# Optimization experiments

Hardware: AMD Instinct MI355X
Metric: run time of the kernel (lower is better)

The kernel has to match this reference:

```python
import jax, jax.numpy as jnp
import numpy as np
from jax import lax

G, NPER, K = 64, 1024, 512          # graphs, nodes per graph, kept per graph (ceil(0.5*1024))
N, E = G * NPER, 1_048_576          # total nodes, total edges
F, H, C = 128, 128, 10              # in_feats, hidden_dim, num_classes


def gcn(x, src, dst, ew, W, b, num_nodes):
    """PyG GCNConv: D^{-1/2}(A+I)D^{-1/2} X W + b, with edge weights ew."""
    xw = x @ W                                              # [N, H]
    deg = jax.ops.segment_sum(ew, dst, num_segments=num_nodes) + 1.0  # +1 self loop
    dinv = lax.rsqrt(deg)
    coef = dinv[src] * dinv[dst] * ew                       # [E]
    agg = jax.ops.segment_sum(coef[:, None] * xw[src], dst, num_segments=num_nodes)
    return agg + (dinv * dinv)[:, None] * xw + b            # self-loop term + bias


def setup_inputs() -> dict:
    key = jax.random.key(0)
    ks = jax.random.split(key, 10)
    x = jax.random.normal(ks[0], (N, F), jnp.float32)
    # intra-graph random edges: dst forced into same graph block as src
    src = jax.random.randint(ks[1], (E,), 0, N, dtype=jnp.int32)
    dst = (src // NPER) * NPER + jax.random.randint(ks[2], (E,), 0, NPER, dtype=jnp.int32)
    edge_index = jnp.stack([src, dst])                      # [2, E]
    batch = jnp.repeat(jnp.arange(G, dtype=jnp.int32), NPER)
    W1 = jax.random.normal(ks[3], (F, H), jnp.float32) / np.sqrt(F)
    b1 = jnp.zeros((H,), jnp.float32)
    p = jax.random.normal(ks[4], (H,), jnp.float32) / np.sqrt(H)   # TopKPooling score vector
    W2 = jax.random.normal(ks[5], (H, H), jnp.float32) / np.sqrt(H)
    b2 = jnp.zeros((H,), jnp.float32)
    Wl = jax.random.normal(ks[6], (H, C), jnp.float32) / np.sqrt(H)
    bl = jnp.zeros((C,), jnp.float32)
    return dict(x=x, edge_index=edge_index, batch=batch, W1=W1, b1=b1, p=p, W2=W2, b2=b2, Wl=Wl, bl=bl)


def reference(x, edge_index, batch, W1, b1, p, W2, b2, Wl, bl):
    src, dst = edge_index[0], edge_index[1]
    ew1 = jnp.ones((E,), x.dtype)
    h = jax.nn.relu(gcn(x, src, dst, ew1, W1, b1, N))       # conv1 + relu

    # --- TopKPooling: score = tanh(x.p/||p||), keep top-K per graph, gate x by score ---
    score = jnp.tanh((h @ p) / jnp.linalg.norm(p))          # [N]
    vals, idx = lax.top_k(score.reshape(G, NPER), K)        # per-graph top-k, [G, K]
    perm = (idx + jnp.arange(G, dtype=idx.dtype)[:, None] * NPER).reshape(-1)  # global ids [G*K]
    h2 = h[perm] * vals.reshape(-1, 1)                      # gated kept nodes [G*K, H]

    # edge re-index: keep only edges with both endpoints surviving (mask via weight 0)
    new_id = jnp.full((N,), -1, jnp.int32).at[perm].set(jnp.arange(G * K, dtype=jnp.int32))
    s2, d2 = new_id[src], new_id[dst]
    mask = (s2 >= 0) & (d2 >= 0)
    ew2 = mask.astype(h.dtype)
    s2 = jnp.where(mask, s2, 0)
    d2 = jnp.where(mask, d2, 0)

    h3 = jax.nn.relu(gcn(h2, s2, d2, ew2, W2, b2, G * K))   # conv2 + relu

    pooled = h3.reshape(G, K, H).mean(axis=1)               # global_mean_pool (equal counts)
    return pooled @ Wl + bl                                 # [G, C]
```

## Files before the change

kernel.cpp:

```cpp
#include <hip/hip_runtime.h>

#define NNODES 65536
#define NEDGES 1048576
#define NGRAPH 64
#define NPERG  1024
#define KEEP   512
#define M2     (NGRAPH * KEEP)
#define HD     128
#define NC     10
#define EMAX   20480

#define OW1 0
#define OW2 16384
#define OWL 32768
#define OB1 34048
#define OB2 34176
#define OP  34304
#define OBL 34432
#define NCVT 34448

typedef __attribute__((ext_vector_type(8))) short bf16x8;
typedef __attribute__((ext_vector_type(4))) float f32x4;

__device__ __forceinline__ float bf2f(unsigned short u) {
    return __uint_as_float(((unsigned int)u) << 16);
}
__device__ __forceinline__ unsigned short f2bf(float f) {
    unsigned int u = __float_as_uint(f);
    unsigned int r = (u + 0x7FFFu + ((u >> 16) & 1u)) >> 16;
    return (unsigned short)r;
}

__global__ __launch_bounds__(256) void prep_kernel(
    const void* __restrict__ W1, const void* __restrict__ b1, const void* __restrict__ p,
    const void* __restrict__ W2, const void* __restrict__ b2, const void* __restrict__ Wl,
    const void* __restrict__ bl, int* __restrict__ flag, float* __restrict__ cw,
    float* __restrict__ invnorm, int* __restrict__ new_id, int* __restrict__ ghist,
    int* __restrict__ gcur0, float* __restrict__ pooled,
    unsigned short* __restrict__ w1t, unsigned short* __restrict__ w2t,
    const int* __restrict__ src, int* __restrict__ phist) {
    int bid = blockIdx.x, t = threadIdx.x;
    const unsigned short* w1u = (const unsigned short*)W1;
    int local = 0;
    for (int i = t; i < 512; i += 256) {
        unsigned short u = w1u[2 * i];
        int e = (u >> 7) & 0xFF;
        local += (e >= 100 && e <= 140) ? 1 : 0;
    }
    __shared__ int red[256];
    __shared__ int lh[NGRAPH];
    red[t] = local;
    __syncthreads();
    for (int off = 128; off; off >>= 1) {
        if (t < off) red[t] += red[t + off];
        __syncthreads();
    }
    int fl = (red[0] >= 384) ? 1 : 0;
    if (bid == 0 && t == 0) flag[0] = fl;

    if (bid < 135) {
        int gid = bid * 256 + t;
        if (gid < NCVT) {
            const void* srcp; int idx;
            if (gid < OB1) {
                if (gid < OW2)      { srcp = W1; idx = gid - OW1; }
                else if (gid < OWL) { srcp = W2; idx = gid - OW2; }
                else                { srcp = Wl; idx = gid - OWL; }
            } else {
                if (gid < OB2)      { srcp = b1; idx = gid - OB1; }
                else if (gid < OP)  { srcp = b2; idx = gid - OB2; }
                else if (gid < OBL) { srcp = p;  idx = gid - OP; }
                else                { srcp = bl; idx = gid - OBL; }
            }
            float v;
            if (gid >= OWL && gid < OB1 && idx >= 1280) v = 0.f;
            else if (gid >= OBL && idx >= NC) v = 0.f;
            else if (fl) v = bf2f(((const unsigned short*)srcp)[idx]);
            else v = ((const float*)srcp)[idx];
            cw[gid] = v;
            if (gid < OW2) {
                int k = gid >> 7, n = gid & 127;
                w1t[n * 128 + k] = f2bf(v);
            } else if (gid < OWL) {
                int r = gid - OW2;
                int k = r >> 7, n = r & 127;
                w2t[n * 128 + k] = f2bf(v);
            }
        }
    } else if (bid == 135) {
        __shared__ float s2a[128];
        float pv = 0.f;
        if (t < 128) pv = fl ? bf2f(((const unsigned short*)p)[t]) : ((const float*)p)[t];
        if (t < 128) s2a[t] = pv * pv;
        __syncthreads();
        for (int off = 64; off; off >>= 1) {
            if (t < off) s2a[t] += s2a[t + off];
            __syncthreads();
        }
        if (t == 0) invnorm[0] = 1.0f / sqrtf(s2a[0]);
    } else if (bid < 392) {
        int i = (bid - 136) * 256 + t;
        new_id[i] = -1;
        if (i < NGRAPH) { ghist[i] = 0; gcur0[i] = 0; }
        if (i < NGRAPH * HD) pooled[i] = 0.f;
    } else {
        if (t < NGRAPH) lh[t] = 0;
        __syncthreads();
        int e0 = (bid - 392) * 4096;
        for (int k = 0; k < 16; k++) atomicAdd(&lh[src[e0 + k * 256 + t] >> 10], 1);
        __syncthreads();
        if (t < NGRAPH) phist[(bid - 392) * 64 + t] = lh[t];
    }
}

__global__ __launch_bounds__(256) void binpass_kernel(const int* __restrict__ src,
                                                      const int* __restrict__ dst,
                                                      const int* __restrict__ phist,
                                                      int* __restrict__ ghist,
                                                      int* __restrict__ gcur0,
                                                      unsigned int* __restrict__ elist) {
    __shared__ int gh[NGRAPH];
    __shared__ int gbS[NGRAPH];
    __shared__ int lh[NGRAPH];
    __shared__ int lbase[NGRAPH];
    __shared__ int qsum[4][NGRAPH];
    int tid = threadIdx.x;
    {
        int g = tid & 63, q = tid >> 6;
        int s = 0;
        for (int b = q * 64; b < q * 64 + 64; b++) s += phist[b * 64 + g];
        qsum[q][g] = s;
    }
    __syncthreads();
    if (tid < NGRAPH) {
        gh[tid] = qsum[0][tid] + qsum[1][tid] + qsum[2][tid] + qsum[3][tid];
        lh[tid] = 0;
        if (blockIdx.x == 0) ghist[tid] = gh[tid];
    }
    __syncthreads();
    if (tid == 0) {
        int s = 0;
        for (int i = 0; i < NGRAPH; i++) { gbS[i] = s; s += gh[i]; }
    }
    __syncthreads();
    int e0 = blockIdx.x * 4096;
    int gs[16]; unsigned int pk[16];
    for (int k = 0; k < 16; k++) {
        int e = e0 + k * 256 + tid;
        int s = src[e], d = dst[e];
        gs[k] = s >> 10;
        pk[k] = (unsigned)(s & 1023) | ((unsigned)(d & 1023) << 10);
        atomicAdd(&lh[gs[k]], 1);
    }
    __syncthreads();
    if (tid < NGRAPH) { lbase[tid] = gbS[tid] + atomicAdd(&gcur0[tid], lh[tid]); lh[tid] = 0; }
    __syncthreads();
    for (int k = 0; k < 16; k++) {
        int g = gs[k];
        int pos = lbase[g] + atomicAdd(&lh[g], 1);
        elist[pos] = pk[k];
    }
}

__global__ __launch_bounds__(1024) void g1csr_kernel(
    const unsigned int* __restrict__ elist, const int* __restrict__ ghist,
    unsigned short* __restrict__ csr16, int* __restrict__ node_base,
    int* __restrict__ deg_out, float* __restrict__ dinv_out,
    const void* __restrict__ Araw, const unsigned short* __restrict__ Wtb,
    unsigned int* __restrict__ Cb, const int* __restrict__ flag) {
    __shared__ unsigned short sc[EMAX];
    __shared__ int cnt[NPERG];
    __shared__ int cur[NPERG];
    __shared__ int wsum[16];
    __shared__ int gh[NGRAPH];
    __shared__ int baseS, nS;
    int bid = blockIdx.x, t = threadIdx.x;
    if (bid < NGRAPH) {
        int g = bid;
        cnt[t] = 0;
        if (t < NGRAPH) gh[t] = ghist[t];
        __syncthreads();
        if (t == 0) {
            int s = 0;
            for (int i = 0; i < g; i++) s += gh[i];
            baseS = s; nS = gh[g];
        }
        __syncthreads();
        int base = baseS;
        int n = nS; if (n > EMAX) n = EMAX;
        for (int j = t; j < n; j += 1024) atomicAdd(&cnt[(elist[base + j] >> 10) & 1023], 1);
        __syncthreads();
        int v = cnt[t];
        int lane = t & 63;
        int x = v;
        for (int off = 1; off < 64; off <<= 1) {
            int y = __shfl_up(x, off);
            if (lane >= off) x += y;
        }
        if (lane == 63) wsum[t >> 6] = x;
        __syncthreads();
        if (t < 16) {
            int wv = wsum[t];
            int wx = wv;
            for (int off = 1; off < 16; off <<= 1) {
                int y = __shfl_up(wx, off);
                if (t >= off) wx += y;
            }
            wsum[t] = wx - wv;
        }
        __syncthreads();
        int excl = x - v + wsum[t >> 6];
        cur[t] = excl;
        deg_out[g * NPERG + t] = v;
        dinv_out[g * NPERG + t] = rsqrtf((float)v + 1.0f);
        node_base[g * NPERG + t] = base + excl;
        __syncthreads();
        for (int j = t; j < n; j += 1024) {
            unsigned int pk = elist[base + j];
            int d = (pk >> 10) & 1023;
            int pos = atomicAdd(&cur[d], 1);
            sc[pos] = (unsigned short)(pk & 1023);
        }
        __syncthreads();
        for (int j = t; j < n; j += 1024) csr16[base + j] = sc[j];
        return;
    }
    int row0 = (bid - NGRAPH) * 256;
    int wave = t >> 6, lane = t & 63;
    int r0 = row0 + wave * 16;
    int row = r0 + (lane & 15);
    int ko = (lane >> 4) * 8;
    f32x4 acc[8];
#pragma unroll
    for (int c = 0; c < 8; c++) acc[c] = (f32x4){0.f, 0.f, 0.f, 0.f};
    bf16x8 afr[4];
    if (flag[0]) {
        const unsigned short* arow = (const unsigned short*)Araw + (size_t)row * HD + ko;
#pragma unroll
        for (int kk = 0; kk < 4; kk++) afr[kk] = *(const bf16x8*)(arow + kk * 32);
    } else {
        const float* arow = (const float*)Araw + (size_t)row * HD + ko;
#pragma unroll
        for (int kk = 0; kk < 4; kk++) {
            float4 f0 = *(const float4*)(arow + kk * 32);
            float4 f1 = *(const float4*)(arow + kk * 32 + 4);
            bf16x8 a;
            a[0] = (short)f2bf(f0.x); a[1] = (short)f2bf(f0.y);
            a[2] = (short)f2bf(f0.z); a[3] = (short)f2bf(f0.w);
            a[4] = (short)f2bf(f1.x); a[5] = (short)f2bf(f1.y);
            a[6] = (short)f2bf(f1.z); a[7] = (short)f2bf(f1.w);
            afr[kk] = a;
        }
    }
    const unsigned short* brow = Wtb + (lane & 15) * HD + ko;
#pragma unroll
    for (int kk = 0; kk < 4; kk++) {
#pragma unroll
        for (int c = 0; c < 8; c++) {
            bf16x8 b = *(const bf16x8*)(brow + c * 16 * HD + kk * 32);
            acc[c] = __builtin_amdgcn_mfma_f32_16x16x32_bf16(afr[kk], b, acc[c], 0, 0, 0);
        }
    }
    int orow0 = r0 + (lane >> 4) * 4;
    bool even = !(lane & 1);
#pragma unroll
    for (int c = 0; c < 8; c++) {
#pragma unroll
        for (int j = 0; j < 4; j++) {
            float v = acc[c][j];
            float pt = __shfl_xor(v, 1);
            if (even) {
                unsigned int u = (unsigned int)f2bf(v) | ((unsigned int)f2bf(pt) << 16);
                Cb[(size_t)(orow0 + j) * 64 + ((c * 16 + (lane & 15)) >> 1)] = u;
            }
        }
    }
}

__global__ __launch_bounds__(256) void s1_pull(const unsigned short* __restrict__ csr16,
                                               const int* __restrict__ node_base,
                                               const int* __restrict__ deg,
                                               const float* __restrict__ dinv,
                                               const unsigned int* __restrict__ xwb,
                                               const float* __restrict__ b1,
                                               const float* __restrict__ pvec,
                                               const float* __restrict__ invnorm,
                                               unsigned int* __restrict__ hb,
                                               float* __restrict__ score) {
    int b = blockIdx.x;
    int xcd = b & 7, j = b >> 3;
    int g = (j >> 8) * 8 + xcd;
    int n = g * NPERG + (j & 255) * 4 + (threadIdx.x >> 6);
    int lane = threadIdx.x & 63;
    int gb = g * NPERG;
    int base = node_base[n], cnt = deg[n];
    int e = 0; float ds = 0.f;
    if (lane < cnt) {
        e = csr16[base + lane];
        ds = dinv[gb + e];
    }
    float a0 = 0.f, a1 = 0.f;
    int klim = cnt < 64 ? cnt : 64;
    int k = 0;
    for (; k + 7 < klim; k += 8) {
        int s0 = __shfl(e, k),     s1 = __shfl(e, k + 1);
        int s2 = __shfl(e, k + 2), s3 = __shfl(e, k + 3);
        int s4 = __shfl(e, k + 4), s5 = __shfl(e, k + 5);
        int s6 = __shfl(e, k + 6), s7 = __shfl(e, k + 7);
        float d0 = __shfl(ds, k),     d1 = __shfl(ds, k + 1);
        float d2 = __shfl(ds, k + 2), d3 = __shfl(ds, k + 3);
        float d4 = __shfl(ds, k + 4), d5 = __shfl(ds, k + 5);
        float d6 = __shfl(ds, k + 6), d7 = __shfl(ds, k + 7);
        unsigned int u0 = xwb[(size_t)(gb + s0) * 64 + lane];
        unsigned int u1 = xwb[(size_t)(gb + s1) * 64 + lane];
        unsigned int u2 = xwb[(size_t)(gb + s2) * 64 + lane];
        unsigned int u3 = xwb[(size_t)(gb + s3) * 64 + lane];
        unsigned int u4 = xwb[(size_t)(gb + s4) * 64 + lane];
        unsigned int u5 = xwb[(size_t)(gb + s5) * 64 + lane];
        unsigned int u6 = xwb[(size_t)(gb + s6) * 64 + lane];
        unsigned int u7 = xwb[(size_t)(gb + s7) * 64 + lane];
        a0 += d0 * __uint_as_float(u0 << 16); a1 += d0 * __uint_as_float(u0 & 0xFFFF0000u);
        a0 += d1 * __uint_as_float(u1 << 16); a1 += d1 * __uint_as_float(u1 & 0xFFFF0000u);
        a0 += d2 * __uint_as_float(u2 << 16); a1 += d2 * __uint_as_float(u2 & 0xFFFF0000u);
        a0 += d3 * __uint_as_float(u3 << 16); a1 += d3 * __uint_as_float(u3 & 0xFFFF0000u);
        a0 += d4 * __uint_as_float(u4 << 16); a1 += d4 * __uint_as_float(u4 & 0xFFFF0000u);
        a0 += d5 * __uint_as_float(u5 << 16); a1 += d5 * __uint_as_float(u5 & 0xFFFF0000u);
        a0 += d6 * __uint_as_float(u6 << 16); a1 += d6 * __uint_as_float(u6 & 0xFFFF0000u);
        a0 += d7 * __uint_as_float(u7 << 16); a1 += d7 * __uint_as_float(u7 & 0xFFFF0000u);
    }
    for (; k + 3 < klim; k += 4) {
        int s0 = __shfl(e, k), s1 = __shfl(e, k + 1);
        int s2 = __shfl(e, k + 2), s3 = __shfl(e, k + 3);
        float d0 = __shfl(ds, k), d1 = __shfl(ds, k + 1);
        float d2 = __shfl(ds, k + 2), d3 = __shfl(ds, k + 3);
        unsigned int u0 = xwb[(size_t)(gb + s0) * 64 + lane];
        unsigned int u1 = xwb[(size_t)(gb + s1) * 64 + lane];
        unsigned int u2 = xwb[(size_t)(gb + s2) * 64 + lane];
        unsigned int u3 = xwb[(size_t)(gb + s3) * 64 + lane];
        a0 += d0 * __uint_as_float(u0 << 16); a1 += d0 * __uint_as_float(u0 & 0xFFFF0000u);
        a0 += d1 * __uint_as_float(u1 << 16); a1 += d1 * __uint_as_float(u1 & 0xFFFF0000u);
        a0 += d2 * __uint_as_float(u2 << 16); a1 += d2 * __uint_as_float(u2 & 0xFFFF0000u);
        a0 += d3 * __uint_as_float(u3 << 16); a1 += d3 * __uint_as_float(u3 & 0xFFFF0000u);
    }
    for (; k < klim; k++) {
        int sk = __shfl(e, k);
        float dk = __shfl(ds, k);
        unsigned int u = xwb[(size_t)(gb + sk) * 64 + lane];
        a0 += dk * __uint_as_float(u << 16); a1 += dk * __uint_as_float(u & 0xFFFF0000u);
    }
    for (; k < cnt; k++) {
        int sk = csr16[base + k];
        float dk = dinv[gb + sk];
        unsigned int u = xwb[(size_t)(gb + sk) * 64 + lane];
        a0 += dk * __uint_as_float(u << 16); a1 += dk * __uint_as_float(u & 0xFFFF0000u);
    }
    float dn = dinv[n];
    float self = dn * dn;
    unsigned int us = xwb[(size_t)n * 64 + lane];
    float2 bb = ((const float2*)b1)[lane];
    float h0 = fmaxf(dn * a0 + self * __uint_as_float(us << 16) + bb.x, 0.f);
    float h1 = fmaxf(dn * a1 + self * __uint_as_float(us & 0xFFFF0000u) + bb.y, 0.f);
    hb[(size_t)n * 64 + lane] = (unsigned int)f2bf(h0) | ((unsigned int)f2bf(h1) << 16);
    float2 pp = ((const float2*)pvec)[lane];
    float sv = h0 * pp.x + h1 * pp.y;
    for (int off = 32; off; off >>= 1) sv += __shfl_down(sv, off);
    if (lane == 0) score[n] = tanhf(sv * invnorm[0]);
}

__global__ __launch_bounds__(1024) void topk_kernel(const float* __restrict__ score,
                                                    float* __restrict__ vals,
                                                    int* __restrict__ perm,
                                                    int* __restrict__ new_id) {
    __shared__ float sv[1024];
    __shared__ int si[1024];
    int g = blockIdx.x, t = threadIdx.x;
    float v = score[g * NPERG + t];
    int idx = t;
    for (int k = 2; k <= 1024; k <<= 1) {
        for (int j = k >> 1; j > 0; j >>= 1) {
            bool desc = ((t & k) == 0);
            bool up = (t & j) != 0;
            float vb; int ib;
            if (j >= 64) {
                sv[t] = v; si[t] = idx;
                __syncthreads();
                vb = sv[t ^ j]; ib = si[t ^ j];
                bool cmp = (v > vb) || (v == vb && idx < ib);
                bool keep = up ? (cmp != desc) : (cmp == desc);
                if (!keep) { v = vb; idx = ib; }
                __syncthreads();
            } else {
                vb = __shfl_xor(v, j);
                ib = __shfl_xor(idx, j);
                bool cmp = (v > vb) || (v == vb && idx < ib);
                bool keep = up ? (cmp != desc) : (cmp == desc);
                if (!keep) { v = vb; idx = ib; }
            }
        }
    }
    if (t < KEEP) {
        int node = g * NPERG + idx;
        int slot = g * KEEP + t;
        vals[slot] = v;
        perm[slot] = node;
        new_id[node] = slot;
    }
}

__global__ __launch_bounds__(512) void g2deg_kernel(
    const unsigned int* __restrict__ elist, const int* __restrict__ ghist,
    const int* __restrict__ new_id, float* __restrict__ dinv2,
    const unsigned int* __restrict__ hb, const int* __restrict__ perm,
    const float* __restrict__ vals, const unsigned short* __restrict__ Wtb,
    unsigned int* __restrict__ Cb) {
    __shared__ int d2[KEEP];
    __shared__ int gh[NGRAPH];
    __shared__ int baseS, nS;
    int bid = blockIdx.x, t = threadIdx.x;
    if (bid < NGRAPH) {
        int g = bid;
        if (t < KEEP) d2[t] = 0;
        if (t < NGRAPH) gh[t] = ghist[t];
        __syncthreads();
        if (t == 0) {
            int s = 0;
            for (int i = 0; i < g; i++) s += gh[i];
            baseS = s; nS = gh[g];
        }
        __syncthreads();
        int base = baseS, n = nS;
        int gb = g * NPERG;
        int kb = g * KEEP;
        for (int j = t; j < n; j += 512) {
            unsigned int pk = elist[base + j];
            int s = pk & 1023, d = (pk >> 10) & 1023;
            int ns = new_id[gb + s], nd = new_id[gb + d];
            if (ns >= 0 && nd >= 0) atomicAdd(&d2[nd - kb], 1);
        }
        __syncthreads();
        if (t < KEEP) dinv2[kb + t] = rsqrtf((float)d2[t] + 1.0f);
        return;
    }
    int row0 = (bid - NGRAPH) * 128;
    int wave = t >> 6, lane = t & 63;
    int r0 = row0 + wave * 16;
    int m = r0 + (lane & 15);
    int ko = (lane >> 4) * 8;
    float sc = vals[m];
    const unsigned int* arow = hb + (size_t)perm[m] * 64 + (ko >> 1);
    bf16x8 afr[4];
#pragma unroll
    for (int kk = 0; kk < 4; kk++) {
        uint4 q = *(const uint4*)(arow + kk * 16);
        bf16x8 a;
        a[0] = (short)f2bf(bf2f((unsigned short)q.x) * sc);
        a[1] = (short)f2bf(bf2f((unsigned short)(q.x >> 16)) * sc);
        a[2] = (short)f2bf(bf2f((unsigned short)q.y) * sc);
        a[3] = (short)f2bf(bf2f((unsigned short)(q.y >> 16)) * sc);
        a[4] = (short)f2bf(bf2f((unsigned short)q.z) * sc);
        a[5] = (short)f2bf(bf2f((unsigned short)(q.z >> 16)) * sc);
        a[6] = (short)f2bf(bf2f((unsigned short)q.w) * sc);
        a[7] = (short)f2bf(bf2f((unsigned short)(q.w >> 16)) * sc);
        afr[kk] = a;
    }
    f32x4 acc[8];
#pragma unroll
    for (int c = 0; c < 8; c++) acc[c] = (f32x4){0.f, 0.f, 0.f, 0.f};
    const unsigned short* brow = Wtb + (lane & 15) * HD + ko;
#pragma unroll
    for (int kk = 0; kk < 4; kk++) {
#pragma unroll
        for (int c = 0; c < 8; c++) {
            bf16x8 b = *(const bf16x8*)(brow + c * 16 * HD + kk * 32);
            acc[c] = __builtin_amdgcn_mfma_f32_16x16x32_bf16(afr[kk], b, acc[c], 0, 0, 0);
        }
    }
    int orow0 = r0 + (lane >> 4) * 4;
    bool even = !(lane & 1);
#pragma unroll
    for (int c = 0; c < 8; c++) {
#pragma unroll
        for (int j = 0; j < 4; j++) {
            float v = acc[c][j];
            float pt = __shfl_xor(v, 1);
            if (even) {
                unsigned int u = (unsigned int)f2bf(v) | ((unsigned int)f2bf(pt) << 16);
                Cb[(size_t)(orow0 + j) * 64 + ((c * 16 + (lane & 15)) >> 1)] = u;
            }
        }
    }
}

__global__ __launch_bounds__(256) void s2_pull(const unsigned short* __restrict__ csr16,
                                               const int* __restrict__ node_base,
                                               const int* __restrict__ deg,
                                               const int* __restrict__ perm,
                                               const int* __restrict__ new_id,
                                               const float* __restrict__ dinv2,
                                               const unsigned int* __restrict__ xwb2,
                                               const float* __restrict__ b2,
                                               float* __restrict__ pooled) {
    __shared__ float pr[HD];
    __shared__ int cnk[4][64];
    __shared__ float cds[4][64];
    int tid = threadIdx.x;
    if (tid < HD) pr[tid] = 0.f;
    __syncthreads();
    int b = blockIdx.x;
    int xcd = b & 7, j = b >> 3;
    int g = (j >> 7) * 8 + xcd;
    int wv = tid >> 6;
    int m = g * KEEP + (j & 127) * 4 + wv;
    int lane = tid & 63;
    int node = perm[m];
    int gb = node & ~(NPERG - 1);
    int base = node_base[node], cnt = deg[node];
    int nk = 0; float ds = 0.f;
    if (lane < cnt) {
        int ns = new_id[gb + csr16[base + lane]];
        if (ns >= 0) { nk = ns; ds = dinv2[ns]; }
    }
    unsigned long long msk = __ballot(ds != 0.f);
    int pos = __popcll(msk & ((1ull << lane) - 1ull));
    if (ds != 0.f) { cnk[wv][pos] = nk; cds[wv][pos] = ds; }
    int na = __popcll(msk);
    float a0 = 0.f, a1 = 0.f;
    int k = 0;
    for (; k + 7 < na; k += 8) {
        int s0 = cnk[wv][k],     s1 = cnk[wv][k + 1];
        int s2 = cnk[wv][k + 2], s3 = cnk[wv][k + 3];
        int s4 = cnk[wv][k + 4], s5 = cnk[wv][k + 5];
        int s6 = cnk[wv][k + 6], s7 = cnk[wv][k + 7];
        float d0 = cds[wv][k],     d1 = cds[wv][k + 1];
        float d2 = cds[wv][k + 2], d3 = cds[wv][k + 3];
        float d4 = cds[wv][k + 4], d5 = cds[wv][k + 5];
        float d6 = cds[wv][k + 6], d7 = cds[wv][k + 7];
        unsigned int u0 = xwb2[(size_t)s0 * 64 + lane];
        unsigned int u1 = xwb2[(size_t)s1 * 64 + lane];
        unsigned int u2 = xwb2[(size_t)s2 * 64 + lane];
        unsigned int u3 = xwb2[(size_t)s3 * 64 + lane];
        unsigned int u4 = xwb2[(size_t)s4 * 64 + lane];
        unsigned int u5 = xwb2[(size_t)s5 * 64 + lane];
        unsigned int u6 = xwb2[(size_t)s6 * 64 + lane];
        unsigned int u7 = xwb2[(size_t)s7 * 64 + lane];
        a0 += d0 * __uint_as_float(u0 << 16); a1 += d0 * __uint_as_float(u0 & 0xFFFF0000u);
        a0 += d1 * __uint_as_float(u1 << 16); a1 += d1 * __uint_as_float(u1 & 0xFFFF0000u);
        a0 += d2 * __uint_as_float(u2 << 16); a1 += d2 * __uint_as_float(u2 & 0xFFFF0000u);
        a0 += d3 * __uint_as_float(u3 << 16); a1 += d3 * __uint_as_float(u3 & 0xFFFF0000u);
        a0 += d4 * __uint_as_float(u4 << 16); a1 += d4 * __uint_as_float(u4 & 0xFFFF0000u);
        a0 += d5 * __uint_as_float(u5 << 16); a1 += d5 * __uint_as_float(u5 & 0xFFFF0000u);
        a0 += d6 * __uint_as_float(u6 << 16); a1 += d6 * __uint_as_float(u6 & 0xFFFF0000u);
        a0 += d7 * __uint_as_float(u7 << 16); a1 += d7 * __uint_as_float(u7 & 0xFFFF0000u);
    }
    for (; k + 3 < na; k += 4) {
        int s0 = cnk[wv][k], s1 = cnk[wv][k + 1];
        int s2 = cnk[wv][k + 2], s3 = cnk[wv][k + 3];
        float d0 = cds[wv][k], d1 = cds[wv][k + 1];
        float d2 = cds[wv][k + 2], d3 = cds[wv][k + 3];
        unsigned int u0 = xwb2[(size_t)s0 * 64 + lane];
        unsigned int u1 = xwb2[(size_t)s1 * 64 + lane];
        unsigned int u2 = xwb2[(size_t)s2 * 64 + lane];
        unsigned int u3 = xwb2[(size_t)s3 * 64 + lane];
        a0 += d0 * __uint_as_float(u0 << 16); a1 += d0 * __uint_as_float(u0 & 0xFFFF0000u);
        a0 += d1 * __uint_as_float(u1 << 16); a1 += d1 * __uint_as_float(u1 & 0xFFFF0000u);
        a0 += d2 * __uint_as_float(u2 << 16); a1 += d2 * __uint_as_float(u2 & 0xFFFF0000u);
        a0 += d3 * __uint_as_float(u3 << 16); a1 += d3 * __uint_as_float(u3 & 0xFFFF0000u);
    }
    for (; k < na; k++) {
        int sk = cnk[wv][k];
        float dk = cds[wv][k];
        unsigned int u = xwb2[(size_t)sk * 64 + lane];
        a0 += dk * __uint_as_float(u << 16); a1 += dk * __uint_as_float(u & 0xFFFF0000u);
    }
    for (int kk = 64; kk < cnt; kk++) {
        int ns = new_id[gb + csr16[base + kk]];
        if (ns >= 0) {
            float dk = dinv2[ns];
            unsigned int u = xwb2[(size_t)ns * 64 + lane];
            a0 += dk * __uint_as_float(u << 16); a1 += dk * __uint_as_float(u & 0xFFFF0000u);
        }
    }
    float dn = dinv2[m];
    float self = dn * dn;
    unsigned int us = xwb2[(size_t)m * 64 + lane];
    float2 bb = ((const float2*)b2)[lane];
    float o0 = fmaxf(dn * a0 + self * __uint_as_float(us << 16) + bb.x, 0.f);
    float o1 = fmaxf(dn * a1 + self * __uint_as_float(us & 0xFFFF0000u) + bb.y, 0.f);
    atomicAdd(&pr[lane * 2], o0);
    atomicAdd(&pr[lane * 2 + 1], o1);
    __syncthreads();
    if (tid < HD) atomicAdd(&pooled[g * HD + tid], pr[tid]);
}

__global__ __launch_bounds__(128) void outk_kernel(const float* __restrict__ pooled,
                                                   const float* __restrict__ Wl,
                                                   const float* __restrict__ bl,
                                                   void* __restrict__ outv,
                                                   const int* __restrict__ flag) {
    int g = blockIdx.x, t = threadIdx.x;
    __shared__ float sp[HD];
    sp[t] = pooled[g * HD + t] * (1.0f / KEEP);
    __syncthreads();
    if (t < NC) {
        float acc = bl[t];
        for (int hh = 0; hh < HD; hh++) acc += sp[hh] * Wl[hh * NC + t];
        if (flag[0]) ((unsigned short*)outv)[g * NC + t] = f2bf(acc);
        else         ((float*)outv)[g * NC + t] = acc;
    }
}

extern "C" void kernel_launch(void* const* d_in, const int* in_sizes, int n_in,
                              void* d_out, int out_size, void* d_ws, size_t ws_size,
                              hipStream_t stream) {
    const int* ei   = (const int*)d_in[1];
    const int* srcv = ei;
    const int* dstv = ei + NEDGES;

    char* w = (char*)d_ws;
    const size_t MB = 1u << 20;
    const size_t KB = 1024;
    float* dinv1     = (float*)(w + 0);
    float* score     = (float*)(w + 256 * KB);
    float* vals      = (float*)(w + 512 * KB);
    int*   perm      = (int*)(w + 640 * KB);
    int*   new_id    = (int*)(w + 768 * KB);
    int*   deg1      = (int*)(w + 1024 * KB);
    int*   node_base = (int*)(w + 1280 * KB);
    float* dinv2     = (float*)(w + 1536 * KB);
    float* invnorm   = (float*)(w + 1664 * KB);
    int*   flag      = (int*)(w + 1664 * KB + 64);
    int*   ghist     = (int*)(w + 1664 * KB + 1024);
    int*   gcur0     = (int*)(w + 1664 * KB + 2048);
    float* cw        = (float*)(w + 1700 * KB);
    float* pooled    = (float*)(w + 1840 * KB);
    unsigned short* w1t = (unsigned short*)(w + 1880 * KB);
    unsigned short* w2t = (unsigned short*)(w + 1912 * KB);
    int* phist       = (int*)(w + 1944 * KB);
    unsigned int* xw1b = (unsigned int*)(w + 2 * MB);
    unsigned int* xw2b = (unsigned int*)(w + 18 * MB);
    unsigned int* hb = (unsigned int*)(w + 34 * MB);
    unsigned int* elist    = (unsigned int*)(w + 66 * MB);
    unsigned short* csr16  = (unsigned short*)(w + 70 * MB);

    float* W1f = cw + OW1; float* W2f = cw + OW2; float* Wlf = cw + OWL;
    float* b1f = cw + OB1; float* b2f = cw + OB2; float* pf  = cw + OP;
    float* blf = cw + OBL;
    (void)W1f; (void)W2f;

    prep_kernel<<<648, 256, 0, stream>>>(d_in[3], d_in[4], d_in[5], d_in[6], d_in[7],
                                         d_in[8], d_in[9], flag, cw, invnorm, new_id,
                                         ghist, gcur0, pooled, w1t, w2t, srcv, phist);
    binpass_kernel<<<256, 256, 0, stream>>>(srcv, dstv, phist, ghist, gcur0, elist);
    g1csr_kernel<<<NGRAPH + NNODES / 256, 1024, 0, stream>>>(
        elist, ghist, csr16, node_base, deg1, dinv1, d_in[0], w1t, xw1b, flag);
    s1_pull<<<NNODES / 4, 256, 0, stream>>>(csr16, node_base, deg1, dinv1, xw1b, b1f, pf,
                                            invnorm, hb, score);
    topk_kernel<<<NGRAPH, 1024, 0, stream>>>(score, vals, perm, new_id);
    g2deg_kernel<<<NGRAPH + M2 / 128, 512, 0, stream>>>(
        elist, ghist, new_id, dinv2, hb, perm, vals, w2t, xw2b);
    s2_pull<<<M2 / 4, 256, 0, stream>>>(csr16, node_base, deg1, perm, new_id, dinv2,
                                        xw2b, b2f, pooled);
    outk_kernel<<<NGRAPH, 128, 0, stream>>>(pooled, Wlf, blf, d_out, flag);

    (void)in_sizes; (void)n_in; (void)out_size; (void)ws_size;
}
```

Before: 257.1 us.

## Fuse edge binning into prep kernel with fixed-capacity per-graph edge slots

```diff
diff --git a/kernel.cpp b/kernel.cpp
--- a/kernel.cpp
+++ b/kernel.cpp
@@ -38,7 +38,8 @@
     float* __restrict__ invnorm, int* __restrict__ new_id, int* __restrict__ ghist,
     int* __restrict__ gcur0, float* __restrict__ pooled,
     unsigned short* __restrict__ w1t, unsigned short* __restrict__ w2t,
-    const int* __restrict__ src, int* __restrict__ phist) {
+    const int* __restrict__ src, const int* __restrict__ dst,
+    unsigned int* __restrict__ elist) {
     int bid = blockIdx.x, t = threadIdx.x;
     const unsigned short* w1u = (const unsigned short*)W1;
     int local = 0;
@@ -49,6 +50,7 @@
     }
     __shared__ int red[256];
     __shared__ int lh[NGRAPH];
+    __shared__ int lbase[NGRAPH];
     red[t] = local;
     __syncthreads();
     for (int off = 128; off; off >>= 1) {
@@ -101,64 +103,32 @@
     } else if (bid < 392) {
         int i = (bid - 136) * 256 + t;
         new_id[i] = -1;
-        if (i < NGRAPH) { ghist[i] = 0; gcur0[i] = 0; }
         if (i < NGRAPH * HD) pooled[i] = 0.f;
     } else {
         if (t < NGRAPH) lh[t] = 0;
         __syncthreads();
         int e0 = (bid - 392) * 4096;
-        for (int k = 0; k < 16; k++) atomicAdd(&lh[src[e0 + k * 256 + t] >> 10], 1);
-        __syncthreads();
-        if (t < NGRAPH) phist[(bid - 392) * 64 + t] = lh[t];
-    }
-}
-
-__global__ __launch_bounds__(256) void binpass_kernel(const int* __restrict__ src,
-                                                      const int* __restrict__ dst,
-                                                      const int* __restrict__ phist,
-                                                      int* __restrict__ ghist,
-                                                      int* __restrict__ gcur0,
-                                                      unsigned int* __restrict__ elist) {
-    __shared__ int gh[NGRAPH];
-    __shared__ int gbS[NGRAPH];
-    __shared__ int lh[NGRAPH];
-    __shared__ int lbase[NGRAPH];
-    __shared__ int qsum[4][NGRAPH];
-    int tid = threadIdx.x;
-    {
-        int g = tid & 63, q = tid >> 6;
-        int s = 0;
-        for (int b = q * 64; b < q * 64 + 64; b++) s += phist[b * 64 + g];
-        qsum[q][g] = s;
-    }
-    __syncthreads();
-    if (tid < NGRAPH) {
-        gh[tid] = qsum[0][tid] + qsum[1][tid] + qsum[2][tid] + qsum[3][tid];
-        lh[tid] = 0;
-        if (blockIdx.x == 0) ghist[tid] = gh[tid];
-    }
-    __syncthreads();
-    if (tid == 0) {
-        int s = 0;
-        for (int i = 0; i < NGRAPH; i++) { gbS[i] = s; s += gh[i]; }
-    }
-    __syncthreads();
-    int e0 = blockIdx.x * 4096;
-    int gs[16]; unsigned int pk[16];
-    for (int k = 0; k < 16; k++) {
-        int e = e0 + k * 256 + tid;
-        int s = src[e], d = dst[e];
-        gs[k] = s >> 10;
-        pk[k] = (unsigned)(s & 1023) | ((unsigned)(d & 1023) << 10);
-        atomicAdd(&lh[gs[k]], 1);
-    }
-    __syncthreads();
-    if (tid < NGRAPH) { lbase[tid] = gbS[tid] + atomicAdd(&gcur0[tid], lh[tid]); lh[tid] = 0; }
-    __syncthreads();
-    for (int k = 0; k < 16; k++) {
-        int g = gs[k];
-        int pos = lbase[g] + atomicAdd(&lh[g], 1);
-        elist[pos] = pk[k];
+        int gs[16]; unsigned int pk[16];
+        for (int k = 0; k < 16; k++) {
+            int e = e0 + k * 256 + t;
+            int s = src[e], d = dst[e];
+            gs[k] = s >> 10;
+            pk[k] = (unsigned)(s & 1023) | ((unsigned)(d & 1023) << 10);
+            atomicAdd(&lh[gs[k]], 1);
+        }
+        __syncthreads();
+        if (t < NGRAPH) {
+            int c = lh[t];
+            lbase[t] = atomicAdd(&gcur0[t], c);
+            atomicAdd(&ghist[t], c);
+            lh[t] = 0;
+        }
+        __syncthreads();
+        for (int k = 0; k < 16; k++) {
+            int g = gs[k];
+            int pos = lbase[g] + atomicAdd(&lh[g], 1);
+            if (pos < EMAX) elist[g * EMAX + pos] = pk[k];
+        }
     }
 }
 
@@ -172,22 +142,13 @@
     __shared__ int cnt[NPERG];
     __shared__ int cur[NPERG];
     __shared__ int wsum[16];
-    __shared__ int gh[NGRAPH];
-    __shared__ int baseS, nS;
     int bid = blockIdx.x, t = threadIdx.x;
     if (bid < NGRAPH) {
         int g = bid;
         cnt[t] = 0;
-        if (t < NGRAPH) gh[t] = ghist[t];
-        __syncthreads();
-        if (t == 0) {
-            int s = 0;
-            for (int i = 0; i < g; i++) s += gh[i];
-            baseS = s; nS = gh[g];
-        }
-        __syncthreads();
-        int base = baseS;
-        int n = nS; if (n > EMAX) n = EMAX;
+        __syncthreads();
+        int base = g * EMAX;
+        int n = ghist[g]; if (n > EMAX) n = EMAX;
         for (int j = t; j < n; j += 1024) atomicAdd(&cnt[(elist[base + j] >> 10) & 1023], 1);
         __syncthreads();
         int v = cnt[t];
@@ -414,21 +375,13 @@
     const float* __restrict__ vals, const unsigned short* __restrict__ Wtb,
     unsigned int* __restrict__ Cb) {
     __shared__ int d2[KEEP];
-    __shared__ int gh[NGRAPH];
-    __shared__ int baseS, nS;
     int bid = blockIdx.x, t = threadIdx.x;
     if (bid < NGRAPH) {
         int g = bid;
         if (t < KEEP) d2[t] = 0;
-        if (t < NGRAPH) gh[t] = ghist[t];
-        __syncthreads();
-        if (t == 0) {
-            int s = 0;
-            for (int i = 0; i < g; i++) s += gh[i];
-            baseS = s; nS = gh[g];
-        }
-        __syncthreads();
-        int base = baseS, n = nS;
+        __syncthreads();
+        int base = g * EMAX;
+        int n = ghist[g]; if (n > EMAX) n = EMAX;
         int gb = g * NPERG;
         int kb = g * KEEP;
         for (int j = t; j < n; j += 512) {
@@ -635,22 +588,23 @@
     float* pooled    = (float*)(w + 1840 * KB);
     unsigned short* w1t = (unsigned short*)(w + 1880 * KB);
     unsigned short* w2t = (unsigned short*)(w + 1912 * KB);
-    int* phist       = (int*)(w + 1944 * KB);
     unsigned int* xw1b = (unsigned int*)(w + 2 * MB);
     unsigned int* xw2b = (unsigned int*)(w + 18 * MB);
     unsigned int* hb = (unsigned int*)(w + 34 * MB);
     unsigned int* elist    = (unsigned int*)(w + 66 * MB);
-    unsigned short* csr16  = (unsigned short*)(w + 70 * MB);
+    unsigned short* csr16  = (unsigned short*)(w + 72 * MB);
 
     float* W1f = cw + OW1; float* W2f = cw + OW2; float* Wlf = cw + OWL;
     float* b1f = cw + OB1; float* b2f = cw + OB2; float* pf  = cw + OP;
     float* blf = cw + OBL;
     (void)W1f; (void)W2f;
 
+    hipMemsetAsync(w + 1664 * KB + 1024, 0, 1280 + 256, stream);
+
     prep_kernel<<<648, 256, 0, stream>>>(d_in[3], d_in[4], d_in[5], d_in[6], d_in[7],
                                          d_in[8], d_in[9], flag, cw, invnorm, new_id,
-                                         ghist, gcur0, pooled, w1t, w2t, srcv, phist);
-    binpass_kernel<<<256, 256, 0, stream>>>(srcv, dstv, phist, ghist, gcur0, elist);
+                                         ghist, gcur0, pooled, w1t, w2t, srcv, dstv,
+                                         elist);
     g1csr_kernel<<<NGRAPH + NNODES / 256, 1024, 0, stream>>>(
         elist, ghist, csr16, node_base, deg1, dinv1, d_in[0], w1t, xw1b, flag);
     s1_pull<<<NNODES / 4, 256, 0, stream>>>(csr16, node_base, deg1, dinv1, xw1b, b1f, pf,
```

New measurement: 243.8 us. 1.05x faster.
